# Kernel tuning notes

Hardware: AMD Instinct MI355X
Metric: run time of the kernel (lower is better)

The kernel has to match this reference:

```python
import jax, jax.numpy as jnp
import numpy as np

SCALING = 2.0  # lora alpha / r

def setup_inputs() -> dict:
    key = jax.random.key(0)
    k1, k2, k3, k4, k5 = jax.random.split(key, 5)
    B, S, D_IN, D_OUT, R = 4, 2048, 4096, 4096, 16
    x = jax.random.normal(k1, (B, S, D_IN), dtype=jnp.float32)
    weight = jax.random.normal(k2, (D_OUT, D_IN), dtype=jnp.float32) * 0.02
    lora_A = jax.random.normal(k3, (R, D_IN), dtype=jnp.float32) * (1.0 / np.sqrt(D_IN))
    lora_B = jax.random.normal(k4, (D_OUT, R), dtype=jnp.float32) * 0.02
    bias = jax.random.normal(k5, (D_OUT,), dtype=jnp.float32) * 0.02
    return {"x": x, "weight": weight, "lora_A": lora_A, "lora_B": lora_B, "bias": bias}

def reference(x, weight, lora_A, lora_B, bias):
    # Faithful to the torch module: materialize W + scaling * (B @ A), then F.linear.
    # effective_weight: [d_out, d_in]
    effective_weight = weight + SCALING * (lora_B @ lora_A)
    # F.linear(x, W, b) = x @ W.T + b
    out = jnp.einsum('bsd,od->bso', x, effective_weight) + bias
    return out
```

## Files before the change

### kernel.cpp

```cpp
#include <hip/hip_runtime.h>
#include <hip/hip_bf16.h>
#include <stdint.h>

typedef unsigned short u16;
typedef u16 u16x4 __attribute__((ext_vector_type(4)));
typedef short bf16x8 __attribute__((ext_vector_type(8)));
typedef float f32x4 __attribute__((ext_vector_type(4)));

__device__ __forceinline__ u16 f2bf(float f) {
  union { float f; uint32_t u; } v; v.f = f;
  uint32_t u = v.u;
  return (u16)((u + 0x7fffu + ((u >> 16) & 1u)) >> 16);
}

__global__ __launch_bounds__(256) void aux_kernel(
    const float4* __restrict__ x, u16x4* __restrict__ xb, int n4, int nCvt,
    const float* __restrict__ W, const float* __restrict__ A,
    const float* __restrict__ Bl, u16* __restrict__ Wout, int DIN) {
  if ((int)blockIdx.x < nCvt) {
    int i = blockIdx.x * 256 + threadIdx.x;
    const int stride = nCvt * 256;
    for (; i < n4; i += stride) {
      float4 v = x[i];
      u16x4 o;
      o.x = f2bf(v.x); o.y = f2bf(v.y); o.z = f2bf(v.z); o.w = f2bf(v.w);
      xb[i] = o;
    }
  } else {
    const int n = blockIdx.x - nCvt;
    float bv[16];
#pragma unroll
    for (int r = 0; r < 16; ++r) bv[r] = 2.0f * Bl[n * 16 + r];
    const int iters = DIN / (256 * 4);
    for (int c = 0; c < iters; ++c) {
      const int k = (c * 256 + (int)threadIdx.x) * 4;
      float4 wv = *(const float4*)&W[(size_t)n * DIN + k];
#pragma unroll
      for (int r = 0; r < 16; ++r) {
        const float4 av = *(const float4*)&A[(size_t)r * DIN + k];
        wv.x += bv[r] * av.x;
        wv.y += bv[r] * av.y;
        wv.z += bv[r] * av.z;
        wv.w += bv[r] * av.w;
      }
      u16x4 o;
      o.x = f2bf(wv.x); o.y = f2bf(wv.y); o.z = f2bf(wv.z); o.w = f2bf(wv.w);
      *(u16x4*)&Wout[(size_t)n * DIN + k] = o;
    }
  }
}

#define BM 256
#define BN 256

__global__ __launch_bounds__(512, 2) void gemm256_kernel(
    const u16* __restrict__ A, const u16* __restrict__ B,
    const float* __restrict__ bias, float* __restrict__ C,
    int M, int N, int K) {
  extern __shared__ u16 lds[];

  const int tid  = threadIdx.x;
  const int lane = tid & 63;
  const int wid  = tid >> 6;

  const int nwg = gridDim.x;
  const int cpx = nwg >> 3;
  const int f   = ((int)blockIdx.x & 7) * cpx + ((int)blockIdx.x >> 3);
  const int nbx = N / BN;
  const int bx = f % nbx, by = f / nbx;
  const int bm = by * BM, bn = bx * BN;

  const int wmL = (wid >> 2) * 128;
  const int wnL = (wid & 3) * 64;
  const int lr  = lane & 15;
  const int lk  = lane >> 4;
  const int rslot = ((lk ^ ((lr >> 1) & 3)) << 3);

  const int srow  = tid >> 2;
  const int sslot = (((tid & 3) ^ ((tid >> 3) & 3)) << 3);
  const u16* gA = A + (size_t)(bm + srow) * K + sslot;
  const u16* gB = B + (size_t)(bn + srow) * K + sslot;

  auto stageA = [&](int par, int ks, int kt) {
    u16* d = &lds[(par * 2 + ks) * 8192 + wid * 512];
    const u16* s = gA + kt * 64 + ks * 32;
#pragma unroll
    for (int i = 0; i < 2; ++i)
      __builtin_amdgcn_global_load_lds(
          (__attribute__((address_space(1))) const void*)(s + (size_t)i * 128 * K),
          (__attribute__((address_space(3))) void*)(d + i * 4096), 16, 0, 0);
  };
  auto stageB = [&](int par, int ks, int kt) {
    u16* d = &lds[32768 + (par * 2 + ks) * 8192 + wid * 512];
    const u16* s = gB + kt * 64 + ks * 32;
#pragma unroll
    for (int i = 0; i < 2; ++i)
      __builtin_amdgcn_global_load_lds(
          (__attribute__((address_space(1))) const void*)(s + (size_t)i * 128 * K),
          (__attribute__((address_space(3))) void*)(d + i * 4096), 16, 0, 0);
  };

  f32x4 acc[8][4];
#pragma unroll
  for (int i = 0; i < 8; ++i)
#pragma unroll
    for (int n = 0; n < 4; ++n) acc[i][n] = f32x4{0.f, 0.f, 0.f, 0.f};

  const int NT = K >> 6;
  stageA(0, 0, 0); stageB(0, 0, 0); stageA(0, 1, 0); stageB(0, 1, 0);
  asm volatile("s_waitcnt vmcnt(4)" ::: "memory");
  __builtin_amdgcn_s_barrier();

#define PIN()   asm volatile("" ::: "memory")
#define LGKM0() asm volatile("s_waitcnt lgkmcnt(0)" ::: "memory")
#define VM4()   asm volatile("s_waitcnt vmcnt(4)" ::: "memory")
#define BAR()   __builtin_amdgcn_s_barrier()

  for (int t = 0; t < NT; ++t) {
    const int par = t & 1, npar = par ^ 1;
    const int tn = (t + 1 < NT) ? t + 1 : 0;

    auto ldA = [&](int ks, int mf) -> bf16x8 {
      return *(const bf16x8*)&lds[(par * 2 + ks) * 8192 + (wmL + mf * 16 + lr) * 32 + rslot];
    };
    auto ldB = [&](int ks, int nf) -> bf16x8 {
      return *(const bf16x8*)&lds[32768 + (par * 2 + ks) * 8192 + (wnL + nf * 16 + lr) * 32 + rslot];
    };

    bf16x8 a[4], b0[4], b1[4];

#pragma unroll
    for (int n = 0; n < 4; ++n) b0[n] = ldB(0, n);
#pragma unroll
    for (int i = 0; i < 4; ++i) a[i] = ldA(0, i);
    stageA(npar, 0, tn);
    PIN(); BAR(); LGKM0();
    __builtin_amdgcn_s_setprio(1);
#pragma unroll
    for (int i = 0; i < 4; ++i)
#pragma unroll
      for (int n = 0; n < 4; ++n)
        acc[i][n] = __builtin_amdgcn_mfma_f32_16x16x32_bf16(a[i], b0[n], acc[i][n], 0, 0, 0);
    __builtin_amdgcn_s_setprio(0);
    BAR();

#pragma unroll
    for (int i = 0; i < 4; ++i) a[i] = ldA(0, 4 + i);
    stageB(npar, 0, tn);
    PIN(); BAR(); LGKM0();
    __builtin_amdgcn_s_setprio(1);
#pragma unroll
    for (int i = 0; i < 4; ++i)
#pragma unroll
      for (int n = 0; n < 4; ++n)
        acc[4 + i][n] = __builtin_amdgcn_mfma_f32_16x16x32_bf16(a[i], b0[n], acc[4 + i][n], 0, 0, 0);
    __builtin_amdgcn_s_setprio(0);
    VM4();
    BAR();

#pragma unroll
    for (int n = 0; n < 4; ++n) b1[n] = ldB(1, n);
#pragma unroll
    for (int i = 0; i < 4; ++i) a[i] = ldA(1, i);
    stageA(npar, 1, tn);
    PIN(); BAR(); LGKM0();
    __builtin_amdgcn_s_setprio(1);
#pragma unroll
    for (int i = 0; i < 4; ++i)
#pragma unroll
      for (int n = 0; n < 4; ++n)
        acc[i][n] = __builtin_amdgcn_mfma_f32_16x16x32_bf16(a[i], b1[n], acc[i][n], 0, 0, 0);
    __builtin_amdgcn_s_setprio(0);
    BAR();

#pragma unroll
    for (int i = 0; i < 4; ++i) a[i] = ldA(1, 4 + i);
    stageB(npar, 1, tn);
    PIN(); BAR(); LGKM0();
    __builtin_amdgcn_s_setprio(1);
#pragma unroll
    for (int i = 0; i < 4; ++i)
#pragma unroll
      for (int n = 0; n < 4; ++n)
        acc[4 + i][n] = __builtin_amdgcn_mfma_f32_16x16x32_bf16(a[i], b1[n], acc[4 + i][n], 0, 0, 0);
    __builtin_amdgcn_s_setprio(0);
    VM4();
    BAR();
  }

  asm volatile("s_waitcnt vmcnt(0)" ::: "memory");
  __builtin_amdgcn_s_barrier();

#pragma unroll
  for (int nf = 0; nf < 4; ++nf) {
    const int col = bn + wnL + nf * 16 + lr;
    const float bv = bias[col];
#pragma unroll
    for (int mf = 0; mf < 8; ++mf) {
      const int row = bm + wmL + mf * 16 + lk * 4;
#pragma unroll
      for (int j = 0; j < 4; ++j)
        C[(size_t)(row + j) * N + col] = acc[mf][nf][j] + bv;
    }
  }
#undef PIN
#undef LGKM0
#undef VM4
#undef BAR
}

extern "C" void kernel_launch(void* const* d_in, const int* in_sizes, int n_in,
                              void* d_out, int out_size, void* d_ws, size_t ws_size,
                              hipStream_t stream) {
  const float* x  = (const float*)d_in[0];
  const float* w  = (const float*)d_in[1];
  const float* lA = (const float*)d_in[2];
  const float* lB = (const float*)d_in[3];
  const float* bs = (const float*)d_in[4];
  float* out = (float*)d_out;

  const int DOUT = in_sizes[4];
  const int DIN  = in_sizes[1] / DOUT;
  const int M    = in_sizes[0] / DIN;

  u16* Xb = (u16*)d_ws;
  u16* Wb = Xb + (size_t)M * DIN;

  const int n4 = (M * DIN) / 4;
  const int nCvt = 2048;
  aux_kernel<<<nCvt + DOUT, 256, 0, stream>>>((const float4*)x, (u16x4*)Xb, n4, nCvt,
                                              w, lA, lB, Wb, DIN);

  (void)hipFuncSetAttribute((const void*)gemm256_kernel,
                            hipFuncAttributeMaxDynamicSharedMemorySize, 131072);

  const int nwg = (M / BM) * (DOUT / BN);
  gemm256_kernel<<<nwg, 512, 131072, stream>>>(Xb, Wb, bs, out, M, DOUT, DIN);
}
```

Before: 341.8 us.

## Software-pipeline LDS fragment loads and cut barriers in GEMM main loop

Restructures the bf16 GEMM inner loop so the A/B fragment reads from LDS for the next MFMA block are issued before the current block's MFMAs. Operand registers are double-buffered (aE/aO, b0/b1), and the next tile's first fragments are prefetched at the end of each iteration. Barriers per K-tile drop from eight to two, and the explicit lgkmcnt(0) waits are removed so LDS latency can hide under MFMA work. The cost is more live vector registers, which may add register pressure at two workgroups per CU. Correctness also now depends on the vmcnt/barrier ordering between the staged buffers and the prefetched reads.

```diff
diff --git a/kernel.cpp b/kernel.cpp
--- a/kernel.cpp
+++ b/kernel.cpp
@@ -100,6 +100,13 @@
           (__attribute__((address_space(3))) void*)(d + i * 4096), 16, 0, 0);
   };
 
+  auto ldA = [&](int par, int ks, int mf) -> bf16x8 {
+    return *(const bf16x8*)&lds[(par * 2 + ks) * 8192 + (wmL + mf * 16 + lr) * 32 + rslot];
+  };
+  auto ldB = [&](int par, int ks, int nf) -> bf16x8 {
+    return *(const bf16x8*)&lds[32768 + (par * 2 + ks) * 8192 + (wnL + nf * 16 + lr) * 32 + rslot];
+  };
+
   f32x4 acc[8][4];
 #pragma unroll
   for (int i = 0; i < 8; ++i)
@@ -111,81 +118,70 @@
   asm volatile("s_waitcnt vmcnt(4)" ::: "memory");
   __builtin_amdgcn_s_barrier();
 
-#define PIN()   asm volatile("" ::: "memory")
-#define LGKM0() asm volatile("s_waitcnt lgkmcnt(0)" ::: "memory")
-#define VM4()   asm volatile("s_waitcnt vmcnt(4)" ::: "memory")
-#define BAR()   __builtin_amdgcn_s_barrier()
+  bf16x8 aE[4], aO[4], b0[4], b1[4];
+#pragma unroll
+  for (int n = 0; n < 4; ++n) b0[n] = ldB(0, 0, n);
+#pragma unroll
+  for (int m = 0; m < 4; ++m) aE[m] = ldA(0, 0, m);
+
+#define VM4() asm volatile("s_waitcnt vmcnt(4)" ::: "memory")
+#define BAR() __builtin_amdgcn_s_barrier()
 
   for (int t = 0; t < NT; ++t) {
     const int par = t & 1, npar = par ^ 1;
     const int tn = (t + 1 < NT) ? t + 1 : 0;
 
-    auto ldA = [&](int ks, int mf) -> bf16x8 {
-      return *(const bf16x8*)&lds[(par * 2 + ks) * 8192 + (wmL + mf * 16 + lr) * 32 + rslot];
-    };
-    auto ldB = [&](int ks, int nf) -> bf16x8 {
-      return *(const bf16x8*)&lds[32768 + (par * 2 + ks) * 8192 + (wnL + nf * 16 + lr) * 32 + rslot];
-    };
-
-    bf16x8 a[4], b0[4], b1[4];
-
-#pragma unroll
-    for (int n = 0; n < 4; ++n) b0[n] = ldB(0, n);
-#pragma unroll
-    for (int i = 0; i < 4; ++i) a[i] = ldA(0, i);
     stageA(npar, 0, tn);
-    PIN(); BAR(); LGKM0();
-    __builtin_amdgcn_s_setprio(1);
-#pragma unroll
-    for (int i = 0; i < 4; ++i)
-#pragma unroll
-      for (int n = 0; n < 4; ++n)
-        acc[i][n] = __builtin_amdgcn_mfma_f32_16x16x32_bf16(a[i], b0[n], acc[i][n], 0, 0, 0);
-    __builtin_amdgcn_s_setprio(0);
-    BAR();
-
-#pragma unroll
-    for (int i = 0; i < 4; ++i) a[i] = ldA(0, 4 + i);
+#pragma unroll
+    for (int m = 0; m < 4; ++m) aO[m] = ldA(par, 0, 4 + m);
+    __builtin_amdgcn_s_setprio(1);
+#pragma unroll
+    for (int m = 0; m < 4; ++m)
+#pragma unroll
+      for (int n = 0; n < 4; ++n)
+        acc[m][n] = __builtin_amdgcn_mfma_f32_16x16x32_bf16(aE[m], b0[n], acc[m][n], 0, 0, 0);
+    __builtin_amdgcn_s_setprio(0);
+
     stageB(npar, 0, tn);
-    PIN(); BAR(); LGKM0();
-    __builtin_amdgcn_s_setprio(1);
-#pragma unroll
-    for (int i = 0; i < 4; ++i)
-#pragma unroll
-      for (int n = 0; n < 4; ++n)
-        acc[4 + i][n] = __builtin_amdgcn_mfma_f32_16x16x32_bf16(a[i], b0[n], acc[4 + i][n], 0, 0, 0);
-    __builtin_amdgcn_s_setprio(0);
     VM4();
     BAR();
-
-#pragma unroll
-    for (int n = 0; n < 4; ++n) b1[n] = ldB(1, n);
-#pragma unroll
-    for (int i = 0; i < 4; ++i) a[i] = ldA(1, i);
+#pragma unroll
+    for (int n = 0; n < 4; ++n) b1[n] = ldB(par, 1, n);
+#pragma unroll
+    for (int m = 0; m < 4; ++m) aE[m] = ldA(par, 1, m);
+    __builtin_amdgcn_s_setprio(1);
+#pragma unroll
+    for (int m = 0; m < 4; ++m)
+#pragma unroll
+      for (int n = 0; n < 4; ++n)
+        acc[4 + m][n] = __builtin_amdgcn_mfma_f32_16x16x32_bf16(aO[m], b0[n], acc[4 + m][n], 0, 0, 0);
+    __builtin_amdgcn_s_setprio(0);
+
     stageA(npar, 1, tn);
-    PIN(); BAR(); LGKM0();
-    __builtin_amdgcn_s_setprio(1);
-#pragma unroll
-    for (int i = 0; i < 4; ++i)
-#pragma unroll
-      for (int n = 0; n < 4; ++n)
-        acc[i][n] = __builtin_amdgcn_mfma_f32_16x16x32_bf16(a[i], b1[n], acc[i][n], 0, 0, 0);
-    __builtin_amdgcn_s_setprio(0);
-    BAR();
-
-#pragma unroll
-    for (int i = 0; i < 4; ++i) a[i] = ldA(1, 4 + i);
+#pragma unroll
+    for (int m = 0; m < 4; ++m) aO[m] = ldA(par, 1, 4 + m);
+    __builtin_amdgcn_s_setprio(1);
+#pragma unroll
+    for (int m = 0; m < 4; ++m)
+#pragma unroll
+      for (int n = 0; n < 4; ++n)
+        acc[m][n] = __builtin_amdgcn_mfma_f32_16x16x32_bf16(aE[m], b1[n], acc[m][n], 0, 0, 0);
+    __builtin_amdgcn_s_setprio(0);
+
     stageB(npar, 1, tn);
-    PIN(); BAR(); LGKM0();
-    __builtin_amdgcn_s_setprio(1);
-#pragma unroll
-    for (int i = 0; i < 4; ++i)
-#pragma unroll
-      for (int n = 0; n < 4; ++n)
-        acc[4 + i][n] = __builtin_amdgcn_mfma_f32_16x16x32_bf16(a[i], b1[n], acc[4 + i][n], 0, 0, 0);
-    __builtin_amdgcn_s_setprio(0);
     VM4();
     BAR();
+#pragma unroll
+    for (int n = 0; n < 4; ++n) b0[n] = ldB(npar, 0, n);
+#pragma unroll
+    for (int m = 0; m < 4; ++m) aE[m] = ldA(npar, 0, m);
+    __builtin_amdgcn_s_setprio(1);
+#pragma unroll
+    for (int m = 0; m < 4; ++m)
+#pragma unroll
+      for (int n = 0; n < 4; ++n)
+        acc[4 + m][n] = __builtin_amdgcn_mfma_f32_16x16x32_bf16(aO[m], b1[n], acc[4 + m][n], 0, 0, 0);
+    __builtin_amdgcn_s_setprio(0);
   }
 
   asm volatile("s_waitcnt vmcnt(0)" ::: "memory");
@@ -203,8 +199,6 @@
         C[(size_t)(row + j) * N + col] = acc[mf][nf][j] + bv;
     }
   }
-#undef PIN
-#undef LGKM0
 #undef VM4
 #undef BAR
 }
```

Result: no change. 335.3 us (-1.9%).
